# Optimization experiments

Measured on AMD Instinct MI355X. Metric: run time of the kernel, lower is better.

The kernel has to match this reference:

```python
import jax, jax.numpy as jnp
import numpy as np

EPS = 1.1920929e-07  # torch clamp_probs eps for float32
TEMP = 0.3           # sampler temperature T


def conv1d(x, w, b, pad):
    # x: [B, Cin, L], w: [Cout, Cin, K] -> [B, Cout, L']
    y = jax.lax.conv_general_dilated(x, w, window_strides=(1,), padding=[(pad, pad)],
                                     dimension_numbers=('NCH', 'OIH', 'NCH'))
    return y + b[None, :, None]


def setup_inputs() -> dict:
    key = jax.random.key(0)
    ks = jax.random.split(key, 20)
    B, L, V, E, F, H, K = 512, 512, 100000, 100, 100, 100, 10
    p = lambda i, shape: jax.random.normal(ks[i], shape, jnp.float32) * 0.02
    return {
        'x': jax.random.randint(ks[0], (B, L), 0, V, dtype=jnp.int32),
        'u': jax.random.uniform(ks[1], (B, K, L), dtype=jnp.float32),
        'emb': p(2, (V, E)),
        'conv1_w': p(3, (F, E, 3)), 'conv1_b': p(4, (F,)),
        'gi_w': p(5, (H, F)), 'gi_b': p(6, (H,)),
        'conv2_w': p(7, (H, F, 3)), 'conv2_b': p(8, (H,)),
        'li_w': p(9, (H, H, 3)), 'li_b': p(10, (H,)),
        'conv3_w': p(11, (F, 2 * H, 1)), 'conv3_b': p(12, (F,)),
        'conv4_w': p(13, (1, F, 1)), 'conv4_b': p(14, (1,)),
        'fc1_w': p(15, (H, E)), 'fc1_b': p(16, (H,)),
        'head_w': p(17, (1, H)), 'head_b': p(18, (1,)),
    }


def _ti_logits(e, conv1_w, conv1_b, gi_w, gi_b, conv2_w, conv2_b,
               li_w, li_b, conv3_w, conv3_b, conv4_w, conv4_b):
    relu = jax.nn.relu
    xt = jnp.swapaxes(e, 1, 2)                       # [B, E, L]
    h = relu(conv1d(xt, conv1_w, conv1_b, 1))        # [B, F, L]
    g = relu(h.mean(axis=-1) @ gi_w.T + gi_b)        # [B, H] (AdaptiveAvgPool1d(1))
    loc = relu(conv1d(relu(conv1d(h, conv2_w, conv2_b, 1)), li_w, li_b, 1))  # [B, H, L]
    gexp = jnp.broadcast_to(g[:, :, None], loc.shape)
    z = jnp.concatenate([gexp, loc], axis=1)         # [B, 2H, L]
    z = relu(conv1d(z, conv3_w, conv3_b, 0))
    return conv1d(z, conv4_w, conv4_b, 0)            # [B, 1, L]


def reference(x, u, emb, conv1_w, conv1_b, gi_w, gi_b, conv2_w, conv2_b,
              li_w, li_b, conv3_w, conv3_b, conv4_w, conv4_b,
              fc1_w, fc1_b, head_w, head_b):
    e = emb[x]                                       # [B, L, E] embedding gather
    logits = _ti_logits(e, conv1_w, conv1_b, gi_w, gi_b, conv2_w, conv2_b,
                        li_w, li_b, conv3_w, conv3_b, conv4_w, conv4_b)
    # Gumbel top-k continuous sampling (training path)
    uc = jnp.clip(u, EPS, 1.0 - EPS)
    gumbel = -jnp.log(-jnp.log(uc))                  # [B, K, L]
    noisy = (gumbel + logits) / TEMP                 # logits [B,1,L] broadcasts over K
    csamples = jax.nn.softmax(noisy, axis=-1).max(axis=1)  # [B, L]
    # distil predictor: masked mean pooling + MLP + sigmoid head
    pooled = (e * csamples[:, :, None]).mean(axis=1)  # [B, E]
    h = jax.nn.relu(pooled @ fc1_w.T + fc1_b)
    out = jax.nn.sigmoid(h @ head_w.T + head_b)       # [B, 1]
    return out, csamples
```

## Files before the change

### kernel.cpp

```cpp
#include <hip/hip_runtime.h>
#include <math.h>

#define DEV __device__ __forceinline__

typedef __attribute__((ext_vector_type(8))) short short8;
typedef __attribute__((ext_vector_type(4))) short short4v;
typedef __attribute__((ext_vector_type(4))) float f32x4;
typedef __attribute__((ext_vector_type(2))) unsigned uint2v;

#define SSTR 136
#define ROWB (16 * SSTR * 2)

DEV short f2bf(float f) {
    unsigned u = __builtin_bit_cast(unsigned, f);
    unsigned r = (u + 0x7fffu + ((u >> 16) & 1u)) >> 16;
    return (short)r;
}

#if __has_builtin(__builtin_amdgcn_cvt_pk_bf16_f32)
DEV unsigned pk2bf(float a, float b) {
    auto v = __builtin_amdgcn_cvt_pk_bf16_f32(a, b);
    return __builtin_bit_cast(unsigned, v);
}
#else
DEV unsigned pk2bf(float a, float b) {
    return ((unsigned)(unsigned short)f2bf(a)) |
           (((unsigned)(unsigned short)f2bf(b)) << 16);
}
#endif

DEV float bfu(short s) {
    unsigned u = ((unsigned)(unsigned short)s) << 16;
    return __builtin_bit_cast(float, u);
}

__global__ __launch_bounds__(256) void emb_cvt_kernel(
    const float* __restrict__ emb, short* __restrict__ embT) {
    int t = threadIdx.x;
    int row = blockIdx.x * 8 + (t >> 5);
    int c4 = t & 31;
    if (c4 >= 28) return;
    short4v v = {0, 0, 0, 0};
    if (c4 < 25) {
        f32x4 e = *(const f32x4*)&emb[row * 100 + c4 * 4];
#pragma unroll
        for (int r = 0; r < 4; ++r) v[r] = f2bf(e[r]);
    }
    *(short4v*)&embT[row * 112 + c4 * 4] = v;
}

__global__ __launch_bounds__(64) void pack_all_kernel(
    const float* __restrict__ c1w, const float* __restrict__ c2w,
    const float* __restrict__ liw, const float* __restrict__ c3w,
    short* __restrict__ A1, short* __restrict__ A2,
    short* __restrict__ A3, short* __restrict__ A4) {
    int bx = blockIdx.x;
    const float* w; short* dst; int mode, lbx;
    if (bx < 70)       { w = c1w; dst = A1; mode = 0; lbx = bx; }
    else if (bx < 140) { w = c2w; dst = A2; mode = 0; lbx = bx - 70; }
    else if (bx < 210) { w = liw; dst = A3; mode = 0; lbx = bx - 140; }
    else               { w = c3w; dst = A4; mode = 1; lbx = bx - 210; }
    int lane = threadIdx.x;
    int f = lbx % 7 * 16 + (lane & 15);
    int kb = (lbx / 7) * 32 + (lane >> 4) * 8;
    short8 v;
#pragma unroll
    for (int j = 0; j < 8; ++j) {
        int kk = kb + j;
        float val = 0.f;
        if (f < 100) {
            if (mode == 0) {
                int oct = kk >> 3, dk = oct / 13;
                int c = (oct - 13 * dk) * 8 + (kk & 7);
                if (dk < 3 && c < 100) val = w[(f * 100 + c) * 3 + dk];
            } else {
                if (kk < 100) val = w[f * 200 + 100 + kk];
            }
        }
        v[j] = f2bf(val);
    }
    *(short8*)&dst[(lbx * 64 + lane) * 8] = v;
}

template<int MT, int NT, int MTB, int NTB, bool CLAMPL, bool POOL,
         bool TO_GLOBAL, bool EDGE>
DEV void ctap(const short* __restrict__ Ap, const short* s_src, short* s_dst,
              short* __restrict__ gout, const int* bofs, const int* bofs4,
              const float* __restrict__ bias, int row0l, int l0,
              float* __restrict__ hpart_slot, int lane) {
    const int q = lane >> 4, n = lane & 15;
    const f32x4 z4 = {0.f, 0.f, 0.f, 0.f};
    f32x4 acc[MT][NT];
#pragma unroll
    for (int mt = 0; mt < MT; ++mt) {
        int fb = (MTB + mt) * 16 + q * 4;
        f32x4 bs = (fb < 100) ? *(const f32x4*)&bias[fb] : z4;
#pragma unroll
        for (int nt = 0; nt < NT; ++nt) acc[mt][nt] = bs;
    }
#pragma unroll
    for (int ks = 0; ks < 10; ++ks) {
        short8 a[MT];
#pragma unroll
        for (int mt = 0; mt < MT; ++mt)
            a[mt] = *(const short8*)&Ap[(ks * 448 + (MTB + mt) * 64 + lane) * 8];
        const char* bp = (const char*)s_src + bofs[ks];
        short8 bf[NT];
#pragma unroll
        for (int nt = 0; nt < NT; ++nt) {
            if (CLAMPL && (NTB + nt) == 4)
                bf[nt] = *(const short8*)((const char*)s_src + bofs4[ks]);
            else
                bf[nt] = *(const short8*)(bp + (NTB + nt) * ROWB);
        }
#pragma unroll
        for (int mt = 0; mt < MT; ++mt)
#pragma unroll
            for (int nt = 0; nt < NT; ++nt)
                acc[mt][nt] = __builtin_amdgcn_mfma_f32_16x16x32_bf16(
                    a[mt], bf[nt], acc[mt][nt], 0, 0, 0);
    }
    f32x4 ps[MT];
    if constexpr (POOL) {
#pragma unroll
        for (int mt = 0; mt < MT; ++mt) ps[mt] = z4;
    }
#pragma unroll
    for (int nt = 0; nt < NT; ++nt) {
        const int j = (NTB + nt) * 16 + n;
        const int l = row0l + j;
        bool lok = true;
        if constexpr (EDGE) lok = ((unsigned)l < 512u);
        const bool pok = POOL && (l >= l0) && (l < l0 + 64);
#pragma unroll
        for (int mt = 0; mt < MT; ++mt) {
            const int fb = (MTB + mt) * 16 + q * 4;
            f32x4 v;
#pragma unroll
            for (int r = 0; r < 4; ++r) {
                v[r] = fmaxf(acc[mt][nt][r], 0.f);
                if constexpr (EDGE) v[r] = lok ? v[r] : 0.f;
            }
            if constexpr (POOL) {
                if (pok) {
#pragma unroll
                    for (int r = 0; r < 4; ++r) ps[mt][r] += v[r];
                }
            }
            uint2v pk;
            pk[0] = pk2bf(v[0], v[1]); pk[1] = pk2bf(v[2], v[3]);
            if constexpr (TO_GLOBAL) {
                *(uint2v*)&gout[j * 112 + fb] = pk;
            } else {
                if ((NTB + nt) < 4 || n < 6)
                    *(uint2v*)&s_dst[j * SSTR + fb] = pk;
            }
        }
    }
    if constexpr (POOL) {
#pragma unroll
        for (int mt = 0; mt < MT; ++mt)
#pragma unroll
            for (int off = 1; off <= 8; off <<= 1)
#pragma unroll
                for (int r = 0; r < 4; ++r)
                    ps[mt][r] += __shfl_xor(ps[mt][r], off, 64);
        if (n == 0) {
#pragma unroll
            for (int mt = 0; mt < MT; ++mt)
                *(f32x4*)&hpart_slot[(MTB + mt) * 16 + q * 4] = ps[mt];
        }
    }
}

__global__ __launch_bounds__(256, 4) void fused_conv_kernel(
    const int* __restrict__ xidx, const short* __restrict__ embT,
    const short* __restrict__ A1, const short* __restrict__ A2,
    const short* __restrict__ A3,
    const float* __restrict__ b1, const float* __restrict__ b2,
    const float* __restrict__ b3,
    short* __restrict__ locT, float* __restrict__ hpart) {
    extern __shared__ char smem[];
    short* s_e = (short*)smem;
    short* s_h = (short*)(smem + 72 * SSTR * 2);
    const int tid = threadIdx.x;
    const int b = blockIdx.y, bx = blockIdx.x, l0 = bx * 64;
    const int lane = tid & 63, wv = tid >> 6;
    const int q = lane >> 4, n = lane & 15;

#pragma unroll
    for (int p = 0; p < 5; ++p) {
        int idx = tid + p * 256;
        int j = idx >> 4, c8 = idx & 15;
        if (j < 70 && c8 < 14) {
            int lg = l0 - 3 + j;
            short8 v = {0, 0, 0, 0, 0, 0, 0, 0};
            if (lg >= 0 && lg < 512) {
                int row = xidx[b * 512 + lg];
                v = *(const short8*)&embT[row * 112 + c8 * 8];
            }
            *(short8*)&s_e[j * SSTR + c8 * 8] = v;
        }
    }

    int bofs[10], bofs4[10];
#pragma unroll
    for (int ks = 0; ks < 10; ++ks) {
        int oct = ks * 4 + q;
        int dk = (oct >= 39) ? 3 : (oct >= 26) ? 2 : (oct >= 13) ? 1 : 0;
        int c0 = (oct - 13 * dk) * 8;
        bofs[ks] = ((n + dk) * SSTR + c0) * 2;
        int r4 = 64 + n + dk; if (r4 > 69) r4 = 69;
        bofs4[ks] = (r4 * SSTR + c0) * 2;
    }
    float* hps = hpart + ((b * 8 + bx) * 2 + (wv & 1)) * 112;
    short* gouts = locT + ((size_t)b * 512 + l0) * 112;

    __syncthreads();
    const bool edge = (bx == 0) || (bx == 7);

#define PASS3T(Ap, SRC, DST, BIAS, R0L, PL, E)                                   \
    if (wv == 0)      ctap<4,3,0,0,false,PL,false,E>(Ap,SRC,DST,nullptr,bofs,bofs4,BIAS,R0L,l0,hps,lane); \
    else if (wv == 1) ctap<4,2,0,3,true, PL,false,E>(Ap,SRC,DST,nullptr,bofs,bofs4,BIAS,R0L,l0,hps,lane); \
    else if (wv == 2) ctap<3,3,4,0,false,PL,false,E>(Ap,SRC,DST,nullptr,bofs,bofs4,BIAS,R0L,l0,hps,lane); \
    else              ctap<3,2,4,3,true, PL,false,E>(Ap,SRC,DST,nullptr,bofs,bofs4,BIAS,R0L,l0,hps,lane);

    if (edge) {
        PASS3T(A1, s_e, s_h, b1, l0 - 2, true, true)
        __syncthreads();
        PASS3T(A2, s_h, s_e, b2, l0 - 1, false, true)
    } else {
        PASS3T(A1, s_e, s_h, b1, l0 - 2, true, false)
        __syncthreads();
        PASS3T(A2, s_h, s_e, b2, l0 - 1, false, false)
    }
    __syncthreads();
    if (wv == 0)      ctap<4,2,0,0,false,false,true,false>(A3,s_e,nullptr,gouts,bofs,bofs4,b3,l0,l0,hps,lane);
    else if (wv == 1) ctap<4,2,0,2,false,false,true,false>(A3,s_e,nullptr,gouts,bofs,bofs4,b3,l0,l0,hps,lane);
    else if (wv == 2) ctap<3,2,4,0,false,false,true,false>(A3,s_e,nullptr,gouts,bofs,bofs4,b3,l0,l0,hps,lane);
    else              ctap<3,2,4,2,false,false,true,false>(A3,s_e,nullptr,gouts,bofs,bofs4,b3,l0,l0,hps,lane);
#undef PASS3T
}

template<int MT, int MTB, int NTB, int SLOT>
DEV void c3tile(const short* s_in, float* s_part, const short* __restrict__ A4,
                const float* __restrict__ zg, const float* __restrict__ w4,
                int bb, int lane) {
    const int q = lane >> 4, n = lane & 15;
    const f32x4 z4 = {0.f, 0.f, 0.f, 0.f};
    f32x4 acc[MT][4];
#pragma unroll
    for (int mt = 0; mt < MT; ++mt) {
        int fb = (MTB + mt) * 16 + q * 4;
        f32x4 zgv = *(const f32x4*)&zg[bb * 112 + fb];
#pragma unroll
        for (int nt = 0; nt < 4; ++nt) acc[mt][nt] = zgv;
    }
#pragma unroll
    for (int ks = 0; ks < 4; ++ks) {
        short8 a[MT];
#pragma unroll
        for (int mt = 0; mt < MT; ++mt)
            a[mt] = *(const short8*)&A4[(ks * 448 + (MTB + mt) * 64 + lane) * 8];
        int c0 = (ks * 4 + q) * 8;
        if (c0 > 104) c0 = 104;
        const char* bp = (const char*)(s_in + n * SSTR + c0);
        short8 bf[4];
#pragma unroll
        for (int nt = 0; nt < 4; ++nt)
            bf[nt] = *(const short8*)(bp + (NTB + nt) * ROWB);
#pragma unroll
        for (int mt = 0; mt < MT; ++mt)
#pragma unroll
            for (int nt = 0; nt < 4; ++nt)
                acc[mt][nt] = __builtin_amdgcn_mfma_f32_16x16x32_bf16(
                    a[mt], bf[nt], acc[mt][nt], 0, 0, 0);
    }
#pragma unroll
    for (int nt = 0; nt < 4; ++nt) {
        float part = 0.f;
#pragma unroll
        for (int mt = 0; mt < MT; ++mt) {
            const int fb = (MTB + mt) * 16 + q * 4;
            f32x4 w4v = (fb < 100) ? *(const f32x4*)&w4[fb] : z4;
#pragma unroll
            for (int r = 0; r < 4; ++r)
                part += fmaxf(acc[mt][nt][r], 0.f) * w4v[r];
        }
        part += __shfl_xor(part, 16, 64);
        part += __shfl_xor(part, 32, 64);
        if (q == 0) s_part[SLOT * 128 + (NTB + nt) * 16 + n] = part;
    }
}

__global__ __launch_bounds__(256, 4) void conv3_logits_kernel(
    const short* __restrict__ locT, const short* __restrict__ A4,
    const float* __restrict__ zg, const float* __restrict__ w4,
    const float* __restrict__ b4, float* __restrict__ logits) {
    extern __shared__ char smem[];
    short* s_in = (short*)smem;
    float* s_part = (float*)(smem + 128 * SSTR * 2);
    const int tid = threadIdx.x;
    const int b = blockIdx.y, l0r = blockIdx.x * 128;
    const int lane = tid & 63, wv = tid >> 6;

    {
        short8 tmp[8];
#pragma unroll
        for (int p = 0; p < 8; ++p) {
            int idx = tid + p * 256;
            int j = idx >> 4, c8 = idx & 15;
            if (c8 < 14)
                tmp[p] = *(const short8*)&locT[((size_t)b * 512 + l0r + j) * 112 + c8 * 8];
        }
#pragma unroll
        for (int p = 0; p < 8; ++p) {
            int idx = tid + p * 256;
            int j = idx >> 4, c8 = idx & 15;
            if (c8 < 14)
                *(short8*)&s_in[j * SSTR + c8 * 8] = tmp[p];
        }
    }
    __syncthreads();
    if (wv == 0)      c3tile<4, 0, 0, 0>(s_in, s_part, A4, zg, w4, b, lane);
    else if (wv == 1) c3tile<4, 0, 4, 0>(s_in, s_part, A4, zg, w4, b, lane);
    else if (wv == 2) c3tile<3, 4, 0, 1>(s_in, s_part, A4, zg, w4, b, lane);
    else              c3tile<3, 4, 4, 1>(s_in, s_part, A4, zg, w4, b, lane);
    __syncthreads();
    if (tid < 128)
        logits[b * 512 + l0r + tid] = s_part[tid] + s_part[128 + tid] + b4[0];
}

__global__ __launch_bounds__(128) void pool_gate_kernel(
    const float* __restrict__ hpart, const float* __restrict__ gi_w,
    const float* __restrict__ gi_b, const float* __restrict__ w3,
    const float* __restrict__ b3, float* __restrict__ zg) {
    int b = blockIdx.x, tid = threadIdx.x;
    __shared__ float s_hm[112];
    __shared__ float s_g[100];
    if (tid < 112) {
        float a = 0.f;
#pragma unroll
        for (int s = 0; s < 16; ++s) a += hpart[(b * 16 + s) * 112 + tid];
        s_hm[tid] = a * (1.f / 512.f);
    }
    __syncthreads();
    if (tid < 100) {
        float a = gi_b[tid];
        for (int f = 0; f < 100; ++f) a += s_hm[f] * gi_w[tid * 100 + f];
        s_g[tid] = fmaxf(a, 0.f);
    }
    __syncthreads();
    if (tid < 112) {
        float a = 0.f;
        if (tid < 100) {
            a = b3[tid];
            for (int h = 0; h < 100; ++h) a += s_g[h] * w3[tid * 200 + h];
        }
        zg[b * 112 + tid] = a;
    }
}

__global__ __launch_bounds__(256) void samp_head_kernel(
    const float* __restrict__ u, const float* __restrict__ logits,
    const int* __restrict__ xidx, const short* __restrict__ embT,
    const float* __restrict__ f1w, const float* __restrict__ f1b,
    const float* __restrict__ hw, const float* __restrict__ hb,
    float* __restrict__ cs_out, float* __restrict__ out) {
    const float EPSV = 1.1920929e-07f;
    const float INVT = 1.f / 0.3f;
    int b = blockIdx.x, tid = threadIdx.x;
    int lane = tid & 63, wv = tid >> 6;
    __shared__ float s_logT[512], s_cs[512];
    __shared__ int s_x[512];
    __shared__ float s_csw[4][512];
    __shared__ float s_acc[16][112];
    __shared__ float s_pool[112], s_h2[100], s_fin[4];
    for (int l = tid; l < 512; l += 256) {
        s_logT[l] = logits[b * 512 + l] * INVT;
        s_x[l] = xidx[b * 512 + l];
    }
    __syncthreads();
    const int nk = (wv < 2) ? 3 : 2;
    float csl[8];
#pragma unroll
    for (int i = 0; i < 8; ++i) csl[i] = 0.f;
    float lt[8];
#pragma unroll
    for (int i = 0; i < 8; ++i) lt[i] = s_logT[lane * 8 + i];
    for (int j = 0; j < nk; ++j) {
        int k = wv + 4 * j;
        f32x4 u0 = *(const f32x4*)&u[(b * 10 + k) * 512 + lane * 8];
        f32x4 u1 = *(const f32x4*)&u[(b * 10 + k) * 512 + lane * 8 + 4];
        float nz[8];
#pragma unroll
        for (int i = 0; i < 8; ++i) {
            float vv = (i < 4) ? u0[i] : u1[i - 4];
            vv = fminf(fmaxf(vv, EPSV), 1.f - EPSV);
            nz[i] = -__logf(-__logf(vv)) * INVT + lt[i];
        }
        float m = nz[0];
#pragma unroll
        for (int i = 1; i < 8; ++i) m = fmaxf(m, nz[i]);
#pragma unroll
        for (int off = 1; off <= 32; off <<= 1) m = fmaxf(m, __shfl_xor(m, off, 64));
        float e[8], s = 0.f;
#pragma unroll
        for (int i = 0; i < 8; ++i) { e[i] = __expf(nz[i] - m); s += e[i]; }
#pragma unroll
        for (int off = 1; off <= 32; off <<= 1) s += __shfl_xor(s, off, 64);
        float inv = 1.f / s;
#pragma unroll
        for (int i = 0; i < 8; ++i) csl[i] = fmaxf(csl[i], e[i] * inv);
    }
#pragma unroll
    for (int i = 0; i < 8; ++i) s_csw[wv][lane * 8 + i] = csl[i];
    __syncthreads();
    for (int l = tid; l < 512; l += 256) {
        float c = fmaxf(fmaxf(s_csw[0][l], s_csw[1][l]),
                        fmaxf(s_csw[2][l], s_csw[3][l]));
        s_cs[l] = c;
        cs_out[b * 512 + l] = c;
    }
    __syncthreads();
    int jg = tid >> 4, c8 = tid & 15;
    if (c8 < 14) {
        f32x4 pa = {0.f, 0.f, 0.f, 0.f}, pb = {0.f, 0.f, 0.f, 0.f};
#pragma unroll 4
        for (int l = jg; l < 512; l += 16) {
            int row = s_x[l];
            float cv = s_cs[l];
            short8 e8 = *(const short8*)&embT[(size_t)row * 112 + c8 * 8];
#pragma unroll
            for (int r = 0; r < 4; ++r) {
                pa[r] += cv * bfu(e8[r]);
                pb[r] += cv * bfu(e8[4 + r]);
            }
        }
        *(f32x4*)&s_acc[jg][c8 * 8] = pa;
        *(f32x4*)&s_acc[jg][c8 * 8 + 4] = pb;
    }
    __syncthreads();
    if (tid < 112) {
        float p = 0.f;
#pragma unroll
        for (int g = 0; g < 16; ++g) p += s_acc[g][tid];
        s_pool[tid] = p * (1.f / 512.f);
    }
    __syncthreads();
    if (tid < 100) {
        float a = f1b[tid];
        for (int i = 0; i < 100; ++i) a += s_pool[i] * f1w[tid * 100 + i];
        s_h2[tid] = fmaxf(a, 0.f);
    }
    __syncthreads();
    float v = (tid < 100) ? s_h2[tid] * hw[tid] : 0.f;
#pragma unroll
    for (int off = 32; off >= 1; off >>= 1) v += __shfl_xor(v, off, 64);
    if (lane == 0) s_fin[wv] = v;
    __syncthreads();
    if (tid == 0) {
        float z = s_fin[0] + s_fin[1] + s_fin[2] + s_fin[3] + hb[0];
        out[b] = 1.f / (1.f + __expf(-z));
    }
}

extern "C" void kernel_launch(void* const* d_in, const int* in_sizes, int n_in,
                              void* d_out, int out_size, void* d_ws, size_t ws_size,
                              hipStream_t stream) {
    const int*   x   = (const int*)d_in[0];
    const float* u   = (const float*)d_in[1];
    const float* emb = (const float*)d_in[2];
    const float* c1w = (const float*)d_in[3];
    const float* c1b = (const float*)d_in[4];
    const float* giw = (const float*)d_in[5];
    const float* gib = (const float*)d_in[6];
    const float* c2w = (const float*)d_in[7];
    const float* c2b = (const float*)d_in[8];
    const float* liw = (const float*)d_in[9];
    const float* lib = (const float*)d_in[10];
    const float* c3w = (const float*)d_in[11];
    const float* c3b = (const float*)d_in[12];
    const float* c4w = (const float*)d_in[13];
    const float* c4b = (const float*)d_in[14];
    const float* f1w = (const float*)d_in[15];
    const float* f1b = (const float*)d_in[16];
    const float* hww = (const float*)d_in[17];
    const float* hbb = (const float*)d_in[18];
    float* out = (float*)d_out;

    char* ws = (char*)d_ws;
    short* locT   = (short*)(ws + 0);
    short* embT   = (short*)(ws + 58720256);
    short* A1     = (short*)(ws + 81120256);
    short* A2     = (short*)(ws + 81191936);
    short* A3     = (short*)(ws + 81263616);
    short* A4     = (short*)(ws + 81335296);
    float* zg     = (float*)(ws + 81363968);
    float* logits = (float*)(ws + 81593344);
    float* hpart  = (float*)(ws + 82641920);

    emb_cvt_kernel<<<12500, 256, 0, stream>>>(emb, embT);
    pack_all_kernel<<<238, 64, 0, stream>>>(c1w, c2w, liw, c3w, A1, A2, A3, A4);

    size_t smemA = 2 * 72 * SSTR * 2;
    fused_conv_kernel<<<dim3(8, 512), 256, smemA, stream>>>(
        x, embT, A1, A2, A3, c1b, c2b, lib, locT, hpart);
    pool_gate_kernel<<<512, 128, 0, stream>>>(hpart, giw, gib, c3w, c3b, zg);
    size_t smemB = 128 * SSTR * 2 + 2 * 128 * 4;
    conv3_logits_kernel<<<dim3(4, 512), 256, smemB, stream>>>(
        locT, A4, zg, c4w, c4b, logits);
    samp_head_kernel<<<512, 256, 0, stream>>>(
        u, logits, x, embT, f1w, f1b, hww, hbb, out + 512, out);
}
```

Measured before the change: 266.5 us.

## Loop fused conv over four L-tiles per block with register-prefetched embedding gather

The fused conv kernel now has each block process four consecutive 64-position tiles instead of one, cutting the grid from 8 to 2 blocks per batch row. The embedding gather for the next tile is issued into registers while the current tile computes, double-buffering the gather. The padded LDS stride is replaced by an XOR-swizzled 128-element row layout to avoid bank conflicts while shrinking shared memory. Packed weights are reordered so each lane's k-steps are contiguous. The cost is fewer blocks and more barriers per block, plus higher register pressure from the prefetch buffers.

```diff
diff --git a/kernel.cpp b/kernel.cpp
--- a/kernel.cpp
+++ b/kernel.cpp
@@ -8,8 +8,8 @@
 typedef __attribute__((ext_vector_type(4))) float f32x4;
 typedef __attribute__((ext_vector_type(2))) unsigned uint2v;
 
-#define SSTR 136
-#define ROWB (16 * SSTR * 2)
+#define RS 128
+#define ROWB (16 * RS * 2)
 
 DEV short f2bf(float f) {
     unsigned u = __builtin_bit_cast(unsigned, f);
@@ -32,6 +32,11 @@
 DEV float bfu(short s) {
     unsigned u = ((unsigned)(unsigned short)s) << 16;
     return __builtin_bit_cast(float, u);
+}
+
+DEV void barrier_lgkm() {
+    asm volatile("s_waitcnt lgkmcnt(0)" ::: "memory");
+    __builtin_amdgcn_s_barrier();
 }
 
 __global__ __launch_bounds__(256) void emb_cvt_kernel(
@@ -61,8 +66,10 @@
     else if (bx < 210) { w = liw; dst = A3; mode = 0; lbx = bx - 140; }
     else               { w = c3w; dst = A4; mode = 1; lbx = bx - 210; }
     int lane = threadIdx.x;
-    int f = lbx % 7 * 16 + (lane & 15);
-    int kb = (lbx / 7) * 32 + (lane >> 4) * 8;
+    int fblk = lbx % 7, ksb = lbx / 7;
+    int f = fblk * 16 + (lane & 15);
+    int kb = ksb * 32 + (lane >> 4) * 8;
+    int nks = (mode == 0) ? 10 : 4;
     short8 v;
 #pragma unroll
     for (int j = 0; j < 8; ++j) {
@@ -79,7 +86,7 @@
         }
         v[j] = f2bf(val);
     }
-    *(short8*)&dst[(lbx * 64 + lane) * 8] = v;
+    *(short8*)&dst[((fblk * 64 + lane) * nks + ksb) * 8] = v;
 }
 
 template<int MT, int NT, int MTB, int NTB, bool CLAMPL, bool POOL,
@@ -89,6 +96,7 @@
               const float* __restrict__ bias, int row0l, int l0,
               float* __restrict__ hpart_slot, int lane) {
     const int q = lane >> 4, n = lane & 15;
+    const int skey = n & 7;
     const f32x4 z4 = {0.f, 0.f, 0.f, 0.f};
     f32x4 acc[MT][NT];
 #pragma unroll
@@ -103,7 +111,7 @@
         short8 a[MT];
 #pragma unroll
         for (int mt = 0; mt < MT; ++mt)
-            a[mt] = *(const short8*)&Ap[(ks * 448 + (MTB + mt) * 64 + lane) * 8];
+            a[mt] = *(const short8*)&Ap[(((MTB + mt) * 64 + lane) * 10 + ks) * 8];
         const char* bp = (const char*)s_src + bofs[ks];
         short8 bf[NT];
 #pragma unroll
@@ -152,8 +160,10 @@
             if constexpr (TO_GLOBAL) {
                 *(uint2v*)&gout[j * 112 + fb] = pk;
             } else {
-                if ((NTB + nt) < 4 || n < 6)
-                    *(uint2v*)&s_dst[j * SSTR + fb] = pk;
+                if ((NTB + nt) < 4 || n < 6) {
+                    const int cch = (MTB + mt) * 2 + (q >> 1);
+                    *(uint2v*)&s_dst[j * RS + ((cch ^ skey) << 3) + (q & 1) * 4] = pk;
+                }
             }
         }
     }
@@ -170,6 +180,35 @@
             for (int mt = 0; mt < MT; ++mt)
                 *(f32x4*)&hpart_slot[(MTB + mt) * 16 + q * 4] = ps[mt];
         }
+    }
+}
+
+DEV void issue_stage(short8* sv, const int* s_xidx,
+                     const short* __restrict__ embT, int tid, int bx, int it) {
+#pragma unroll
+    for (int p = 0; p < 5; ++p) {
+        int idx = tid + p * 256;
+        int j = idx >> 4, c8 = idx & 15;
+        short8 v = {0, 0, 0, 0, 0, 0, 0, 0};
+        if (j < 70 && c8 < 14) {
+            int li = it * 64 + j;
+            int lg = bx * 256 + li - 3;
+            if (lg >= 0 && lg < 512) {
+                int row = s_xidx[li];
+                v = *(const short8*)&embT[(size_t)row * 112 + c8 * 8];
+            }
+        }
+        sv[p] = v;
+    }
+}
+
+DEV void write_stage(const short8* sv, short* s_e, int tid) {
+#pragma unroll
+    for (int p = 0; p < 5; ++p) {
+        int idx = tid + p * 256;
+        int j = idx >> 4, c8 = idx & 15;
+        if (j < 70 && c8 < 14)
+            *(short8*)&s_e[j * RS + ((c8 ^ (j & 7)) << 3)] = sv[p];
     }
 }
 
@@ -182,24 +221,19 @@
     short* __restrict__ locT, float* __restrict__ hpart) {
     extern __shared__ char smem[];
     short* s_e = (short*)smem;
-    short* s_h = (short*)(smem + 72 * SSTR * 2);
+    short* s_h = (short*)(smem + 72 * RS * 2);
+    int* s_xidx = (int*)(smem + 2 * 72 * RS * 2);
     const int tid = threadIdx.x;
-    const int b = blockIdx.y, bx = blockIdx.x, l0 = bx * 64;
+    const int b = blockIdx.y, bx = blockIdx.x;
     const int lane = tid & 63, wv = tid >> 6;
     const int q = lane >> 4, n = lane & 15;
 
-#pragma unroll
-    for (int p = 0; p < 5; ++p) {
-        int idx = tid + p * 256;
-        int j = idx >> 4, c8 = idx & 15;
-        if (j < 70 && c8 < 14) {
-            int lg = l0 - 3 + j;
-            short8 v = {0, 0, 0, 0, 0, 0, 0, 0};
-            if (lg >= 0 && lg < 512) {
-                int row = xidx[b * 512 + lg];
-                v = *(const short8*)&embT[row * 112 + c8 * 8];
-            }
-            *(short8*)&s_e[j * SSTR + c8 * 8] = v;
+    {
+        int g = bx * 256 - 3 + tid;
+        s_xidx[tid] = ((unsigned)g < 512u) ? xidx[b * 512 + g] : 0;
+        if (tid < 8) {
+            int i2 = 256 + tid, g2 = bx * 256 - 3 + i2;
+            s_xidx[i2] = ((unsigned)g2 < 512u) ? xidx[b * 512 + g2] : 0;
         }
     }
 
@@ -208,38 +242,56 @@
     for (int ks = 0; ks < 10; ++ks) {
         int oct = ks * 4 + q;
         int dk = (oct >= 39) ? 3 : (oct >= 26) ? 2 : (oct >= 13) ? 1 : 0;
-        int c0 = (oct - 13 * dk) * 8;
-        bofs[ks] = ((n + dk) * SSTR + c0) * 2;
+        int c = oct - 13 * dk;
+        int r = n + dk;
+        bofs[ks] = (r * RS + ((c ^ (r & 7)) << 3)) * 2;
         int r4 = 64 + n + dk; if (r4 > 69) r4 = 69;
-        bofs4[ks] = (r4 * SSTR + c0) * 2;
-    }
-    float* hps = hpart + ((b * 8 + bx) * 2 + (wv & 1)) * 112;
-    short* gouts = locT + ((size_t)b * 512 + l0) * 112;
-
-    __syncthreads();
-    const bool edge = (bx == 0) || (bx == 7);
-
-#define PASS3T(Ap, SRC, DST, BIAS, R0L, PL, E)                                   \
+        bofs4[ks] = (r4 * RS + ((c ^ (r4 & 7)) << 3)) * 2;
+    }
+
+    barrier_lgkm();
+    short8 svA[5], svB[5];
+    issue_stage(svA, s_xidx, embT, tid, bx, 0);
+
+#define PASS12(Ap, SRC, DST, BIAS, R0L, PL, E)                                   \
     if (wv == 0)      ctap<4,3,0,0,false,PL,false,E>(Ap,SRC,DST,nullptr,bofs,bofs4,BIAS,R0L,l0,hps,lane); \
     else if (wv == 1) ctap<4,2,0,3,true, PL,false,E>(Ap,SRC,DST,nullptr,bofs,bofs4,BIAS,R0L,l0,hps,lane); \
     else if (wv == 2) ctap<3,3,4,0,false,PL,false,E>(Ap,SRC,DST,nullptr,bofs,bofs4,BIAS,R0L,l0,hps,lane); \
     else              ctap<3,2,4,3,true, PL,false,E>(Ap,SRC,DST,nullptr,bofs,bofs4,BIAS,R0L,l0,hps,lane);
 
-    if (edge) {
-        PASS3T(A1, s_e, s_h, b1, l0 - 2, true, true)
-        __syncthreads();
-        PASS3T(A2, s_h, s_e, b2, l0 - 1, false, true)
-    } else {
-        PASS3T(A1, s_e, s_h, b1, l0 - 2, true, false)
-        __syncthreads();
-        PASS3T(A2, s_h, s_e, b2, l0 - 1, false, false)
-    }
-    __syncthreads();
-    if (wv == 0)      ctap<4,2,0,0,false,false,true,false>(A3,s_e,nullptr,gouts,bofs,bofs4,b3,l0,l0,hps,lane);
-    else if (wv == 1) ctap<4,2,0,2,false,false,true,false>(A3,s_e,nullptr,gouts,bofs,bofs4,b3,l0,l0,hps,lane);
-    else if (wv == 2) ctap<3,2,4,0,false,false,true,false>(A3,s_e,nullptr,gouts,bofs,bofs4,b3,l0,l0,hps,lane);
-    else              ctap<3,2,4,2,false,false,true,false>(A3,s_e,nullptr,gouts,bofs,bofs4,b3,l0,l0,hps,lane);
-#undef PASS3T
+    for (int it = 0; it < 4; ++it) {
+        if ((it & 1) == 0) {
+            write_stage(svA, s_e, tid);
+            if (it < 3) issue_stage(svB, s_xidx, embT, tid, bx, it + 1);
+        } else {
+            write_stage(svB, s_e, tid);
+            if (it < 3) issue_stage(svA, s_xidx, embT, tid, bx, it + 1);
+        }
+        barrier_lgkm();
+
+        const int t = bx * 4 + it;
+        const int l0 = t * 64;
+        float* hps = hpart + ((b * 16 + t * 2) + (wv & 1)) * 112;
+        short* gouts = locT + ((size_t)b * 512 + l0) * 112;
+        const bool edge = (t == 0) || (t == 7);
+
+        if (edge) {
+            PASS12(A1, s_e, s_h, b1, l0 - 2, true, true)
+            barrier_lgkm();
+            PASS12(A2, s_h, s_e, b2, l0 - 1, false, true)
+        } else {
+            PASS12(A1, s_e, s_h, b1, l0 - 2, true, false)
+            barrier_lgkm();
+            PASS12(A2, s_h, s_e, b2, l0 - 1, false, false)
+        }
+        barrier_lgkm();
+        if (wv == 0)      ctap<4,2,0,0,false,false,true,false>(A3,s_e,nullptr,gouts,bofs,bofs4,b3,l0,l0,hps,lane);
+        else if (wv == 1) ctap<4,2,0,2,false,false,true,false>(A3,s_e,nullptr,gouts,bofs,bofs4,b3,l0,l0,hps,lane);
+        else if (wv == 2) ctap<3,2,4,0,false,false,true,false>(A3,s_e,nullptr,gouts,bofs,bofs4,b3,l0,l0,hps,lane);
+        else              ctap<3,2,4,2,false,false,true,false>(A3,s_e,nullptr,gouts,bofs,bofs4,b3,l0,l0,hps,lane);
+        barrier_lgkm();
+    }
+#undef PASS12
 }
 
 template<int MT, int MTB, int NTB, int SLOT>
@@ -261,10 +313,10 @@
         short8 a[MT];
 #pragma unroll
         for (int mt = 0; mt < MT; ++mt)
-            a[mt] = *(const short8*)&A4[(ks * 448 + (MTB + mt) * 64 + lane) * 8];
-        int c0 = (ks * 4 + q) * 8;
-        if (c0 > 104) c0 = 104;
-        const char* bp = (const char*)(s_in + n * SSTR + c0);
+            a[mt] = *(const short8*)&A4[(((MTB + mt) * 64 + lane) * 4 + ks) * 8];
+        int cc = ks * 4 + q;
+        if (cc > 13) cc = 13;
+        const char* bp = (const char*)(s_in + n * RS + ((cc ^ (n & 7)) << 3));
         short8 bf[4];
 #pragma unroll
         for (int nt = 0; nt < 4; ++nt)
@@ -299,7 +351,7 @@
     const float* __restrict__ b4, float* __restrict__ logits) {
     extern __shared__ char smem[];
     short* s_in = (short*)smem;
-    float* s_part = (float*)(smem + 128 * SSTR * 2);
+    float* s_part = (float*)(smem + 128 * RS * 2);
     const int tid = threadIdx.x;
     const int b = blockIdx.y, l0r = blockIdx.x * 128;
     const int lane = tid & 63, wv = tid >> 6;
@@ -318,7 +370,7 @@
             int idx = tid + p * 256;
             int j = idx >> 4, c8 = idx & 15;
             if (c8 < 14)
-                *(short8*)&s_in[j * SSTR + c8 * 8] = tmp[p];
+                *(short8*)&s_in[j * RS + ((c8 ^ (j & 7)) << 3)] = tmp[p];
         }
     }
     __syncthreads();
@@ -503,11 +555,11 @@
     emb_cvt_kernel<<<12500, 256, 0, stream>>>(emb, embT);
     pack_all_kernel<<<238, 64, 0, stream>>>(c1w, c2w, liw, c3w, A1, A2, A3, A4);
 
-    size_t smemA = 2 * 72 * SSTR * 2;
-    fused_conv_kernel<<<dim3(8, 512), 256, smemA, stream>>>(
+    size_t smemA = (size_t)2 * 72 * RS * 2 + 264 * 4;
+    fused_conv_kernel<<<dim3(2, 512), 256, smemA, stream>>>(
         x, embT, A1, A2, A3, c1b, c2b, lib, locT, hpart);
     pool_gate_kernel<<<512, 128, 0, stream>>>(hpart, giw, gib, c3w, c3b, zg);
-    size_t smemB = 128 * SSTR * 2 + 2 * 128 * 4;
+    size_t smemB = (size_t)128 * RS * 2 + 2 * 128 * 4;
     conv3_logits_kernel<<<dim3(4, 512), 256, smemB, stream>>>(
         locT, A4, zg, c4w, c4b, logits);
     samp_head_kernel<<<512, 256, 0, stream>>>(
```

After: 1.018 ms. 3.82x slower.

## Load LDS tiles via global_load_lds with XOR-swizzled rows and repack weights

Applied to the files above, without the earlier changes.

Embedding and locT tiles now go straight from global memory into shared memory with global_load_lds, instead of passing through registers. The padded row stride of 136 is replaced by an unpadded 128-short stride with an XOR swizzle, which avoids bank conflicts without the padding. Edge rows outside the sequence are zeroed after the load rather than skipped. Packed weights are laid out so each lane's k-slices sit next to each other, and conv3's launch bound drops to 2 blocks per SM. The direct loads read past the 112-element rows into padding or neighbouring data that is never used.

```diff
diff --git a/kernel.cpp b/kernel.cpp
--- a/kernel.cpp
+++ b/kernel.cpp
@@ -8,8 +8,8 @@
 typedef __attribute__((ext_vector_type(4))) float f32x4;
 typedef __attribute__((ext_vector_type(2))) unsigned uint2v;
 
-#define SSTR 136
-#define ROWB (16 * SSTR * 2)
+#define RS 128
+#define ROWB (16 * RS * 2)
 
 DEV short f2bf(float f) {
     unsigned u = __builtin_bit_cast(unsigned, f);
@@ -32,6 +32,12 @@
 DEV float bfu(short s) {
     unsigned u = ((unsigned)(unsigned short)s) << 16;
     return __builtin_bit_cast(float, u);
+}
+
+DEV void gl_lds16(const void* gsrc, void* ldst) {
+    __builtin_amdgcn_global_load_lds(
+        (const __attribute__((address_space(1))) void*)gsrc,
+        (__attribute__((address_space(3))) void*)ldst, 16, 0, 0);
 }
 
 __global__ __launch_bounds__(256) void emb_cvt_kernel(
@@ -61,8 +67,10 @@
     else if (bx < 210) { w = liw; dst = A3; mode = 0; lbx = bx - 140; }
     else               { w = c3w; dst = A4; mode = 1; lbx = bx - 210; }
     int lane = threadIdx.x;
-    int f = lbx % 7 * 16 + (lane & 15);
-    int kb = (lbx / 7) * 32 + (lane >> 4) * 8;
+    int fblk = lbx % 7, ksb = lbx / 7;
+    int f = fblk * 16 + (lane & 15);
+    int kb = ksb * 32 + (lane >> 4) * 8;
+    int nks = (mode == 0) ? 10 : 4;
     short8 v;
 #pragma unroll
     for (int j = 0; j < 8; ++j) {
@@ -79,7 +87,7 @@
         }
         v[j] = f2bf(val);
     }
-    *(short8*)&dst[(lbx * 64 + lane) * 8] = v;
+    *(short8*)&dst[((fblk * 64 + lane) * nks + ksb) * 8] = v;
 }
 
 template<int MT, int NT, int MTB, int NTB, bool CLAMPL, bool POOL,
@@ -89,6 +97,7 @@
               const float* __restrict__ bias, int row0l, int l0,
               float* __restrict__ hpart_slot, int lane) {
     const int q = lane >> 4, n = lane & 15;
+    const int skey = n & 7;
     const f32x4 z4 = {0.f, 0.f, 0.f, 0.f};
     f32x4 acc[MT][NT];
 #pragma unroll
@@ -103,7 +112,7 @@
         short8 a[MT];
 #pragma unroll
         for (int mt = 0; mt < MT; ++mt)
-            a[mt] = *(const short8*)&Ap[(ks * 448 + (MTB + mt) * 64 + lane) * 8];
+            a[mt] = *(const short8*)&Ap[(((MTB + mt) * 64 + lane) * 10 + ks) * 8];
         const char* bp = (const char*)s_src + bofs[ks];
         short8 bf[NT];
 #pragma unroll
@@ -152,8 +161,10 @@
             if constexpr (TO_GLOBAL) {
                 *(uint2v*)&gout[j * 112 + fb] = pk;
             } else {
-                if ((NTB + nt) < 4 || n < 6)
-                    *(uint2v*)&s_dst[j * SSTR + fb] = pk;
+                if ((NTB + nt) < 4 || n < 6) {
+                    const int cch = (MTB + mt) * 2 + (q >> 1);
+                    *(uint2v*)&s_dst[j * RS + ((cch ^ skey) << 3) + (q & 1) * 4] = pk;
+                }
             }
         }
     }
@@ -182,24 +193,27 @@
     short* __restrict__ locT, float* __restrict__ hpart) {
     extern __shared__ char smem[];
     short* s_e = (short*)smem;
-    short* s_h = (short*)(smem + 72 * SSTR * 2);
+    short* s_h = (short*)(smem + 72 * RS * 2);
     const int tid = threadIdx.x;
     const int b = blockIdx.y, bx = blockIdx.x, l0 = bx * 64;
     const int lane = tid & 63, wv = tid >> 6;
     const int q = lane >> 4, n = lane & 15;
 
-#pragma unroll
-    for (int p = 0; p < 5; ++p) {
-        int idx = tid + p * 256;
-        int j = idx >> 4, c8 = idx & 15;
-        if (j < 70 && c8 < 14) {
-            int lg = l0 - 3 + j;
-            short8 v = {0, 0, 0, 0, 0, 0, 0, 0};
-            if (lg >= 0 && lg < 512) {
-                int row = xidx[b * 512 + lg];
-                v = *(const short8*)&embT[row * 112 + c8 * 8];
-            }
-            *(short8*)&s_e[j * SSTR + c8 * 8] = v;
+    {
+        const int jr = tid >> 4;
+        const int g = (tid & 15) ^ (jr & 7);
+        int rows[5];
+#pragma unroll
+        for (int p = 0; p < 5; ++p) {
+            int lg = l0 - 3 + jr + p * 16;
+            int lgc = lg < 0 ? 0 : (lg > 511 ? 511 : lg);
+            rows[p] = xidx[b * 512 + lgc];
+        }
+#pragma unroll
+        for (int p = 0; p < 5; ++p) {
+            if (wv * 4 + p * 16 < 72)
+                gl_lds16(&embT[(size_t)rows[p] * 112 + g * 8],
+                         &s_e[(wv * 4 + p * 16) * RS]);
         }
     }
 
@@ -208,16 +222,25 @@
     for (int ks = 0; ks < 10; ++ks) {
         int oct = ks * 4 + q;
         int dk = (oct >= 39) ? 3 : (oct >= 26) ? 2 : (oct >= 13) ? 1 : 0;
-        int c0 = (oct - 13 * dk) * 8;
-        bofs[ks] = ((n + dk) * SSTR + c0) * 2;
+        int c = oct - 13 * dk;
+        int r = n + dk;
+        bofs[ks] = (r * RS + ((c ^ (r & 7)) << 3)) * 2;
         int r4 = 64 + n + dk; if (r4 > 69) r4 = 69;
-        bofs4[ks] = (r4 * SSTR + c0) * 2;
+        bofs4[ks] = (r4 * RS + ((c ^ (r4 & 7)) << 3)) * 2;
     }
     float* hps = hpart + ((b * 8 + bx) * 2 + (wv & 1)) * 112;
     short* gouts = locT + ((size_t)b * 512 + l0) * 112;
 
     __syncthreads();
     const bool edge = (bx == 0) || (bx == 7);
+    if (edge) {
+        if (tid < 48) {
+            int row = (bx == 0 ? 0 : 67) + (tid >> 4);
+            short8 z = {0, 0, 0, 0, 0, 0, 0, 0};
+            *(short8*)&s_e[row * RS + (tid & 15) * 8] = z;
+        }
+        __syncthreads();
+    }
 
 #define PASS3T(Ap, SRC, DST, BIAS, R0L, PL, E)                                   \
     if (wv == 0)      ctap<4,3,0,0,false,PL,false,E>(Ap,SRC,DST,nullptr,bofs,bofs4,BIAS,R0L,l0,hps,lane); \
@@ -261,10 +284,10 @@
         short8 a[MT];
 #pragma unroll
         for (int mt = 0; mt < MT; ++mt)
-            a[mt] = *(const short8*)&A4[(ks * 448 + (MTB + mt) * 64 + lane) * 8];
-        int c0 = (ks * 4 + q) * 8;
-        if (c0 > 104) c0 = 104;
-        const char* bp = (const char*)(s_in + n * SSTR + c0);
+            a[mt] = *(const short8*)&A4[(((MTB + mt) * 64 + lane) * 4 + ks) * 8];
+        int cc = ks * 4 + q;
+        if (cc > 13) cc = 13;
+        const char* bp = (const char*)(s_in + n * RS + ((cc ^ (n & 7)) << 3));
         short8 bf[4];
 #pragma unroll
         for (int nt = 0; nt < 4; ++nt)
@@ -293,32 +316,26 @@
     }
 }
 
-__global__ __launch_bounds__(256, 4) void conv3_logits_kernel(
+__global__ __launch_bounds__(256, 2) void conv3_logits_kernel(
     const short* __restrict__ locT, const short* __restrict__ A4,
     const float* __restrict__ zg, const float* __restrict__ w4,
     const float* __restrict__ b4, float* __restrict__ logits) {
     extern __shared__ char smem[];
     short* s_in = (short*)smem;
-    float* s_part = (float*)(smem + 128 * SSTR * 2);
+    float* s_part = (float*)(smem + 128 * RS * 2);
     const int tid = threadIdx.x;
     const int b = blockIdx.y, l0r = blockIdx.x * 128;
     const int lane = tid & 63, wv = tid >> 6;
 
     {
-        short8 tmp[8];
+        const int jr = tid >> 4;
+        const int g = (tid & 15) ^ (jr & 7);
+        const size_t rowbase = (size_t)b * 512 + l0r;
 #pragma unroll
         for (int p = 0; p < 8; ++p) {
-            int idx = tid + p * 256;
-            int j = idx >> 4, c8 = idx & 15;
-            if (c8 < 14)
-                tmp[p] = *(const short8*)&locT[((size_t)b * 512 + l0r + j) * 112 + c8 * 8];
-        }
-#pragma unroll
-        for (int p = 0; p < 8; ++p) {
-            int idx = tid + p * 256;
-            int j = idx >> 4, c8 = idx & 15;
-            if (c8 < 14)
-                *(short8*)&s_in[j * SSTR + c8 * 8] = tmp[p];
+            int j = jr + p * 16;
+            gl_lds16(&locT[(rowbase + j) * 112 + g * 8],
+                     &s_in[(wv * 4 + p * 16) * RS]);
         }
     }
     __syncthreads();
@@ -503,11 +520,11 @@
     emb_cvt_kernel<<<12500, 256, 0, stream>>>(emb, embT);
     pack_all_kernel<<<238, 64, 0, stream>>>(c1w, c2w, liw, c3w, A1, A2, A3, A4);
 
-    size_t smemA = 2 * 72 * SSTR * 2;
+    size_t smemA = (size_t)2 * 72 * RS * 2;
     fused_conv_kernel<<<dim3(8, 512), 256, smemA, stream>>>(
         x, embT, A1, A2, A3, c1b, c2b, lib, locT, hpart);
     pool_gate_kernel<<<512, 128, 0, stream>>>(hpart, giw, gib, c3w, c3b, zg);
-    size_t smemB = 128 * SSTR * 2 + 2 * 128 * 4;
+    size_t smemB = (size_t)128 * RS * 2 + 2 * 128 * 4;
     conv3_logits_kernel<<<dim3(4, 512), 256, smemB, stream>>>(
         locT, A4, zg, c4w, c4b, logits);
     samp_head_kernel<<<512, 256, 0, stream>>>(
```

After: 561.3 us. 2.11x slower.

## Split conv MFMA tiles across waves by output channel, repack weights ks-contiguous

Applied to the files above, without the earlier changes.

Waves in the fused conv kernel now each own a slice of output-channel tiles and cover all sequence tiles, instead of the old mixed M/N split. Each wave therefore reads a disjoint part of the packed weights, and the pooled partial sums no longer need two slots per block. The conv3 kernel is reorganised the same way: each wave owns all seven channel tiles and two position tiles, which removes the cross-wave slot reduction and half of the partial-sum shared memory. Packed weights are relaid so each lane's k-step fragments sit next to each other, aiming for more contiguous global loads. The trade-off is more LDS B-fragment reads per wave, higher accumulator register pressure, and an uneven last wave that has only one channel tile.

```diff
diff --git a/kernel.cpp b/kernel.cpp
--- a/kernel.cpp
+++ b/kernel.cpp
@@ -61,8 +61,10 @@
     else if (bx < 210) { w = liw; dst = A3; mode = 0; lbx = bx - 140; }
     else               { w = c3w; dst = A4; mode = 1; lbx = bx - 210; }
     int lane = threadIdx.x;
-    int f = lbx % 7 * 16 + (lane & 15);
-    int kb = (lbx / 7) * 32 + (lane >> 4) * 8;
+    int fblk = lbx % 7, ksb = lbx / 7;
+    int f = fblk * 16 + (lane & 15);
+    int kb = ksb * 32 + (lane >> 4) * 8;
+    int nks = (mode == 0) ? 10 : 4;
     short8 v;
 #pragma unroll
     for (int j = 0; j < 8; ++j) {
@@ -79,7 +81,7 @@
         }
         v[j] = f2bf(val);
     }
-    *(short8*)&dst[(lbx * 64 + lane) * 8] = v;
+    *(short8*)&dst[((fblk * 64 + lane) * nks + ksb) * 8] = v;
 }
 
 template<int MT, int NT, int MTB, int NTB, bool CLAMPL, bool POOL,
@@ -103,7 +105,7 @@
         short8 a[MT];
 #pragma unroll
         for (int mt = 0; mt < MT; ++mt)
-            a[mt] = *(const short8*)&Ap[(ks * 448 + (MTB + mt) * 64 + lane) * 8];
+            a[mt] = *(const short8*)&Ap[(((MTB + mt) * 64 + lane) * 10 + ks) * 8];
         const char* bp = (const char*)s_src + bofs[ks];
         short8 bf[NT];
 #pragma unroll
@@ -213,17 +215,17 @@
         int r4 = 64 + n + dk; if (r4 > 69) r4 = 69;
         bofs4[ks] = (r4 * SSTR + c0) * 2;
     }
-    float* hps = hpart + ((b * 8 + bx) * 2 + (wv & 1)) * 112;
+    float* hps = hpart + (b * 8 + bx) * 112;
     short* gouts = locT + ((size_t)b * 512 + l0) * 112;
 
     __syncthreads();
     const bool edge = (bx == 0) || (bx == 7);
 
 #define PASS3T(Ap, SRC, DST, BIAS, R0L, PL, E)                                   \
-    if (wv == 0)      ctap<4,3,0,0,false,PL,false,E>(Ap,SRC,DST,nullptr,bofs,bofs4,BIAS,R0L,l0,hps,lane); \
-    else if (wv == 1) ctap<4,2,0,3,true, PL,false,E>(Ap,SRC,DST,nullptr,bofs,bofs4,BIAS,R0L,l0,hps,lane); \
-    else if (wv == 2) ctap<3,3,4,0,false,PL,false,E>(Ap,SRC,DST,nullptr,bofs,bofs4,BIAS,R0L,l0,hps,lane); \
-    else              ctap<3,2,4,3,true, PL,false,E>(Ap,SRC,DST,nullptr,bofs,bofs4,BIAS,R0L,l0,hps,lane);
+    if (wv == 0)      ctap<2,5,0,0,true,PL,false,E>(Ap,SRC,DST,nullptr,bofs,bofs4,BIAS,R0L,l0,hps,lane); \
+    else if (wv == 1) ctap<2,5,2,0,true,PL,false,E>(Ap,SRC,DST,nullptr,bofs,bofs4,BIAS,R0L,l0,hps,lane); \
+    else if (wv == 2) ctap<2,5,4,0,true,PL,false,E>(Ap,SRC,DST,nullptr,bofs,bofs4,BIAS,R0L,l0,hps,lane); \
+    else              ctap<1,5,6,0,true,PL,false,E>(Ap,SRC,DST,nullptr,bofs,bofs4,BIAS,R0L,l0,hps,lane);
 
     if (edge) {
         PASS3T(A1, s_e, s_h, b1, l0 - 2, true, true)
@@ -235,53 +237,53 @@
         PASS3T(A2, s_h, s_e, b2, l0 - 1, false, false)
     }
     __syncthreads();
-    if (wv == 0)      ctap<4,2,0,0,false,false,true,false>(A3,s_e,nullptr,gouts,bofs,bofs4,b3,l0,l0,hps,lane);
-    else if (wv == 1) ctap<4,2,0,2,false,false,true,false>(A3,s_e,nullptr,gouts,bofs,bofs4,b3,l0,l0,hps,lane);
-    else if (wv == 2) ctap<3,2,4,0,false,false,true,false>(A3,s_e,nullptr,gouts,bofs,bofs4,b3,l0,l0,hps,lane);
-    else              ctap<3,2,4,2,false,false,true,false>(A3,s_e,nullptr,gouts,bofs,bofs4,b3,l0,l0,hps,lane);
+    if (wv == 0)      ctap<2,4,0,0,false,false,true,false>(A3,s_e,nullptr,gouts,bofs,bofs4,b3,l0,l0,hps,lane);
+    else if (wv == 1) ctap<2,4,2,0,false,false,true,false>(A3,s_e,nullptr,gouts,bofs,bofs4,b3,l0,l0,hps,lane);
+    else if (wv == 2) ctap<2,4,4,0,false,false,true,false>(A3,s_e,nullptr,gouts,bofs,bofs4,b3,l0,l0,hps,lane);
+    else              ctap<1,4,6,0,false,false,true,false>(A3,s_e,nullptr,gouts,bofs,bofs4,b3,l0,l0,hps,lane);
 #undef PASS3T
 }
 
-template<int MT, int MTB, int NTB, int SLOT>
+template<int NTB>
 DEV void c3tile(const short* s_in, float* s_part, const short* __restrict__ A4,
                 const float* __restrict__ zg, const float* __restrict__ w4,
                 int bb, int lane) {
     const int q = lane >> 4, n = lane & 15;
     const f32x4 z4 = {0.f, 0.f, 0.f, 0.f};
-    f32x4 acc[MT][4];
-#pragma unroll
-    for (int mt = 0; mt < MT; ++mt) {
-        int fb = (MTB + mt) * 16 + q * 4;
+    f32x4 acc[7][2];
+#pragma unroll
+    for (int mt = 0; mt < 7; ++mt) {
+        int fb = mt * 16 + q * 4;
         f32x4 zgv = *(const f32x4*)&zg[bb * 112 + fb];
 #pragma unroll
-        for (int nt = 0; nt < 4; ++nt) acc[mt][nt] = zgv;
+        for (int nt = 0; nt < 2; ++nt) acc[mt][nt] = zgv;
     }
 #pragma unroll
     for (int ks = 0; ks < 4; ++ks) {
-        short8 a[MT];
-#pragma unroll
-        for (int mt = 0; mt < MT; ++mt)
-            a[mt] = *(const short8*)&A4[(ks * 448 + (MTB + mt) * 64 + lane) * 8];
+        short8 a[7];
+#pragma unroll
+        for (int mt = 0; mt < 7; ++mt)
+            a[mt] = *(const short8*)&A4[((mt * 64 + lane) * 4 + ks) * 8];
         int c0 = (ks * 4 + q) * 8;
         if (c0 > 104) c0 = 104;
         const char* bp = (const char*)(s_in + n * SSTR + c0);
-        short8 bf[4];
-#pragma unroll
-        for (int nt = 0; nt < 4; ++nt)
+        short8 bf[2];
+#pragma unroll
+        for (int nt = 0; nt < 2; ++nt)
             bf[nt] = *(const short8*)(bp + (NTB + nt) * ROWB);
 #pragma unroll
-        for (int mt = 0; mt < MT; ++mt)
-#pragma unroll
-            for (int nt = 0; nt < 4; ++nt)
+        for (int mt = 0; mt < 7; ++mt)
+#pragma unroll
+            for (int nt = 0; nt < 2; ++nt)
                 acc[mt][nt] = __builtin_amdgcn_mfma_f32_16x16x32_bf16(
                     a[mt], bf[nt], acc[mt][nt], 0, 0, 0);
     }
 #pragma unroll
-    for (int nt = 0; nt < 4; ++nt) {
+    for (int nt = 0; nt < 2; ++nt) {
         float part = 0.f;
 #pragma unroll
-        for (int mt = 0; mt < MT; ++mt) {
-            const int fb = (MTB + mt) * 16 + q * 4;
+        for (int mt = 0; mt < 7; ++mt) {
+            const int fb = mt * 16 + q * 4;
             f32x4 w4v = (fb < 100) ? *(const f32x4*)&w4[fb] : z4;
 #pragma unroll
             for (int r = 0; r < 4; ++r)
@@ -289,7 +291,7 @@
         }
         part += __shfl_xor(part, 16, 64);
         part += __shfl_xor(part, 32, 64);
-        if (q == 0) s_part[SLOT * 128 + (NTB + nt) * 16 + n] = part;
+        if (q == 0) s_part[(NTB + nt) * 16 + n] = part;
     }
 }
 
@@ -322,13 +324,13 @@
         }
     }
     __syncthreads();
-    if (wv == 0)      c3tile<4, 0, 0, 0>(s_in, s_part, A4, zg, w4, b, lane);
-    else if (wv == 1) c3tile<4, 0, 4, 0>(s_in, s_part, A4, zg, w4, b, lane);
-    else if (wv == 2) c3tile<3, 4, 0, 1>(s_in, s_part, A4, zg, w4, b, lane);
-    else              c3tile<3, 4, 4, 1>(s_in, s_part, A4, zg, w4, b, lane);
+    if (wv == 0)      c3tile<0>(s_in, s_part, A4, zg, w4, b, lane);
+    else if (wv == 1) c3tile<2>(s_in, s_part, A4, zg, w4, b, lane);
+    else if (wv == 2) c3tile<4>(s_in, s_part, A4, zg, w4, b, lane);
+    else              c3tile<6>(s_in, s_part, A4, zg, w4, b, lane);
     __syncthreads();
     if (tid < 128)
-        logits[b * 512 + l0r + tid] = s_part[tid] + s_part[128 + tid] + b4[0];
+        logits[b * 512 + l0r + tid] = s_part[tid] + b4[0];
 }
 
 __global__ __launch_bounds__(128) void pool_gate_kernel(
@@ -341,7 +343,7 @@
     if (tid < 112) {
         float a = 0.f;
 #pragma unroll
-        for (int s = 0; s < 16; ++s) a += hpart[(b * 16 + s) * 112 + tid];
+        for (int s = 0; s < 8; ++s) a += hpart[(b * 8 + s) * 112 + tid];
         s_hm[tid] = a * (1.f / 512.f);
     }
     __syncthreads();
@@ -507,7 +509,7 @@
     fused_conv_kernel<<<dim3(8, 512), 256, smemA, stream>>>(
         x, embT, A1, A2, A3, c1b, c2b, lib, locT, hpart);
     pool_gate_kernel<<<512, 128, 0, stream>>>(hpart, giw, gib, c3w, c3b, zg);
-    size_t smemB = 128 * SSTR * 2 + 2 * 128 * 4;
+    size_t smemB = 128 * SSTR * 2 + 128 * 4;
     conv3_logits_kernel<<<dim3(4, 512), 256, smemB, stream>>>(
         locT, A4, zg, c4w, c4b, logits);
     samp_head_kernel<<<512, 256, 0, stream>>>(
```

Result: slower. 366.6 us (+37.6%).
